# Kernel optimization log

Hardware: AMD Instinct MI355X
Metric: run time of the kernel (lower is better)

The kernel has to match this reference:

```python
import jax, jax.numpy as jnp
import numpy as np

VOCAB, EMBED, HIDDEN, T = 50257, 512, 1024, 2048

def setup_inputs() -> dict:
    key = jax.random.key(0)
    ks = jax.random.split(key, 7)
    s_e = 1.0 / np.sqrt(EMBED)
    s_h = 1.0 / np.sqrt(HIDDEN)
    return {
        "x": jax.random.randint(ks[0], (T,), 0, VOCAB),
        "emb": jax.random.normal(ks[1], (VOCAB, EMBED), dtype=jnp.float32),
        "W_xh": jax.random.uniform(ks[2], (HIDDEN, EMBED), minval=-s_e, maxval=s_e, dtype=jnp.float32),
        "W_hh": jax.random.uniform(ks[3], (HIDDEN, HIDDEN), minval=-s_h, maxval=s_h, dtype=jnp.float32),
        "b_hh": jax.random.uniform(ks[4], (HIDDEN,), minval=-s_h, maxval=s_h, dtype=jnp.float32),
        "W_out": jax.random.uniform(ks[5], (VOCAB, HIDDEN), minval=-s_h, maxval=s_h, dtype=jnp.float32),
        "b_out": jax.random.uniform(ks[6], (VOCAB,), minval=-s_h, maxval=s_h, dtype=jnp.float32),
    }

def reference(x, emb, W_xh, W_hh, b_hh, W_out, b_out):
    # embeds: [T, E]; precompute input projections for all steps (batched GEMM)
    embeds = emb[x]                      # [T, E]
    xp = embeds @ W_xh.T                 # [T, H]

    def step(h, xp_t):
        # h: [H]; nonlinear recurrence must be sequential
        h_new = jnp.tanh(xp_t + h @ W_hh.T + b_hh)
        return h_new, h_new

    h0 = jnp.zeros((HIDDEN,), dtype=xp.dtype)
    h_final, hs = jax.lax.scan(step, h0, xp)   # hs: [T, H]
    logits = hs @ W_out.T + b_out               # [T, VOCAB]
    return logits, h_final[None, :]
```

## Files before the change

### kernel.cpp

```cpp
#include <hip/hip_runtime.h>
#include <hip/hip_bf16.h>

#define VOCAB 50257
#define EMBED 512
#define HIDDEN 1024
#define TSEQ 2048
#define NPAD 50304
#define LOGITS_SIZE ((size_t)TSEQ * VOCAB)

#define OFF_XP   ((size_t)0)
#define OFF_HS   ((size_t)(TSEQ * HIDDEN * 4))
#define OFF_HP   (OFF_HS + (size_t)TSEQ * HIDDEN * 2)
#define OFF_WB   (OFF_HP + 16384 + 256)
#define WS_NEED_FULL (OFF_WB + (size_t)NPAD * HIDDEN * 2)

typedef short bf16x8 __attribute__((ext_vector_type(8)));
typedef float f32x4  __attribute__((ext_vector_type(4)));
typedef short short8 __attribute__((ext_vector_type(8)));

static __device__ __forceinline__ unsigned short f2bf(float f) {
    unsigned u = __float_as_uint(f);
    unsigned r = (u + 0x7fffu + ((u >> 16) & 1u)) >> 16;
    return (unsigned short)r;
}

__global__ __launch_bounds__(256, 2) void emb_xp_kernel(
    const int* __restrict__ x, const float* __restrict__ emb,
    const float* __restrict__ Wxh, float* __restrict__ xp)
{
    __shared__ float As[64][68];
    __shared__ float Bs[64][68];
    __shared__ int   xs[64];
    const int tid = threadIdx.x;
    const int t0 = blockIdx.y * 64, j0 = blockIdx.x * 64;
    if (tid < 64) xs[tid] = x[t0 + tid];
    __syncthreads();
    const int ty = tid >> 4, tx = tid & 15;
    float acc[4][4] = {};
    for (int kc = 0; kc < EMBED; kc += 64) {
        __syncthreads();
#pragma unroll
        for (int i = 0; i < 4; ++i) {
            int s = i * 256 + tid;
            int r = s >> 4, c4 = s & 15;
            *(float4*)&As[r][c4 * 4] = *(const float4*)&emb[(size_t)xs[r] * EMBED + kc + c4 * 4];
            *(float4*)&Bs[r][c4 * 4] = *(const float4*)&Wxh[(size_t)(j0 + r) * EMBED + kc + c4 * 4];
        }
        __syncthreads();
        for (int kk = 0; kk < 64; ++kk) {
            float a[4], b[4];
#pragma unroll
            for (int u = 0; u < 4; ++u) a[u] = As[ty + 16 * u][kk];
#pragma unroll
            for (int v = 0; v < 4; ++v) b[v] = Bs[tx + 16 * v][kk];
#pragma unroll
            for (int u = 0; u < 4; ++u)
#pragma unroll
                for (int v = 0; v < 4; ++v) acc[u][v] += a[u] * b[v];
        }
    }
#pragma unroll
    for (int u = 0; u < 4; ++u)
#pragma unroll
        for (int v = 0; v < 4; ++v)
            xp[(size_t)(t0 + ty + 16 * u) * HIDDEN + j0 + tx + 16 * v] = acc[u][v];
}

__global__ void conv_wout_kernel(const float* __restrict__ W, unsigned short* __restrict__ Wb)
{
    size_t i = (size_t)blockIdx.x * blockDim.x + threadIdx.x;
    size_t idx = i * 4;
    if (idx >= (size_t)NPAD * HIDDEN) return;
    size_t row = idx >> 10;
    float4 v = make_float4(0.f, 0.f, 0.f, 0.f);
    if (row < VOCAB) v = *(const float4*)&W[idx];
    ushort4 o = make_ushort4(f2bf(v.x), f2bf(v.y), f2bf(v.z), f2bf(v.w));
    *(ushort4*)&Wb[idx] = o;
}

#define RNN_WGS 256
__global__ __launch_bounds__(64, 1) void rnn_recur_kernel(
    const float* __restrict__ xp, const float* __restrict__ Whh,
    const float* __restrict__ bhh, unsigned long long* hpair ,
    unsigned short* __restrict__ hs_bf16, float* __restrict__ h_final)
{
    const int tid = threadIdx.x;
    const int j = blockIdx.x * 4 + (tid >> 4);
    const int k16 = tid & 15;

    float4 w4[16];
#pragma unroll
    for (int ii = 0; ii < 16; ++ii)
        w4[ii] = *(const float4*)&Whh[(size_t)j * HIDDEN + ii * 64 + k16 * 4];
#pragma unroll
    for (int ii = 0; ii < 16; ++ii)
        asm volatile("" : "+v"(w4[ii].x), "+v"(w4[ii].y), "+v"(w4[ii].z), "+v"(w4[ii].w));
    const float bj = bhh[j];

#pragma unroll 1
    for (int t = 0; t < TSEQ; ++t) {
        unsigned long long* hin  = hpair + ((t & 1) << 10);
        unsigned long long* hout = hpair + (((t + 1) & 1) << 10);
        const float xpv = xp[(size_t)t * HIDDEN + j];

        float hvf[64];
        for (;;) {
            int mn = 0x7fffffff;
#pragma unroll
            for (int ii = 0; ii < 16; ++ii) {
#pragma unroll
                for (int c = 0; c < 4; ++c) {
                    unsigned long long v = __hip_atomic_load(
                        &hin[ii * 64 + k16 * 4 + c],
                        __ATOMIC_RELAXED, __HIP_MEMORY_SCOPE_AGENT);
                    int tag = (int)(unsigned)(v >> 32);
                    mn = tag < mn ? tag : mn;
                    hvf[ii * 4 + c] = __uint_as_float((unsigned)v);
                }
            }
            if (__all(mn >= t)) break;
        }

        float sum = 0.f;
#pragma unroll
        for (int ii = 0; ii < 16; ++ii)
            sum += w4[ii].x * hvf[ii * 4 + 0] + w4[ii].y * hvf[ii * 4 + 1]
                 + w4[ii].z * hvf[ii * 4 + 2] + w4[ii].w * hvf[ii * 4 + 3];
        sum += __shfl_xor(sum, 1);
        sum += __shfl_xor(sum, 2);
        sum += __shfl_xor(sum, 4);
        sum += __shfl_xor(sum, 8);

        const float val = tanhf(sum + bj + xpv);
        if (k16 == 0) {
            unsigned long long pk = ((unsigned long long)(unsigned)(t + 1) << 32)
                                  | (unsigned long long)__float_as_uint(val);
            __hip_atomic_store(&hout[j], pk, __ATOMIC_RELAXED, __HIP_MEMORY_SCOPE_AGENT);
            hs_bf16[(size_t)t * HIDDEN + j] = f2bf(val);
            if (t == TSEQ - 1) h_final[j] = val;
        }
    }
}

template <bool PRE>
__global__ __launch_bounds__(256, 2) void out_gemm_kernel(
    const unsigned short* __restrict__ hs,
    const unsigned short* __restrict__ Wb,
    const float* __restrict__ Wf,
    const float* __restrict__ b_out,
    float* __restrict__ out)
{
    __shared__ short As[128 * 32];
    __shared__ short Bs[128 * 32];
    const int tid = threadIdx.x;
    const int wid = tid >> 6, lane = tid & 63;
    const int wm = wid >> 1, wn = wid & 1;
    const int l15 = lane & 15, quad = lane >> 4;
    const int m0 = blockIdx.y * 128, n0 = blockIdx.x * 128;

    f32x4 acc[4][4];
#pragma unroll
    for (int a = 0; a < 4; ++a)
#pragma unroll
        for (int b = 0; b < 4; ++b) acc[a][b] = (f32x4){0.f, 0.f, 0.f, 0.f};

    for (int k0 = 0; k0 < HIDDEN; k0 += 32) {
        __syncthreads();
#pragma unroll
        for (int i = 0; i < 2; ++i) {
            int ss = i * 256 + tid;
            int r = ss >> 2, c = ss & 3;
            short8 av = *(const short8*)(hs + (size_t)(m0 + r) * HIDDEN + k0 + c * 8);
            *(short8*)&As[r * 32 + c * 8] = av;
        }
        if (PRE) {
#pragma unroll
            for (int i = 0; i < 2; ++i) {
                int ss = i * 256 + tid;
                int r = ss >> 2, c = ss & 3;
                short8 bv = *(const short8*)(Wb + (size_t)(n0 + r) * HIDDEN + k0 + c * 8);
                *(short8*)&Bs[r * 32 + c * 8] = bv;
            }
        } else {
#pragma unroll
            for (int i = 0; i < 4; ++i) {
                int ss = i * 256 + tid;
                int r = ss >> 3, c4 = ss & 7;
                float4 v = make_float4(0.f, 0.f, 0.f, 0.f);
                if (n0 + r < VOCAB) v = *(const float4*)&Wf[(size_t)(n0 + r) * HIDDEN + k0 + c4 * 4];
                ushort4 u = make_ushort4(f2bf(v.x), f2bf(v.y), f2bf(v.z), f2bf(v.w));
                *(ushort4*)&Bs[r * 32 + c4 * 4] = u;
            }
        }
        __syncthreads();

        bf16x8 af[4], bfr[4];
#pragma unroll
        for (int mi = 0; mi < 4; ++mi)
            af[mi] = *(const bf16x8*)&As[(wm * 64 + mi * 16 + l15) * 32 + quad * 8];
#pragma unroll
        for (int ni = 0; ni < 4; ++ni)
            bfr[ni] = *(const bf16x8*)&Bs[(wn * 64 + ni * 16 + l15) * 32 + quad * 8];
#pragma unroll
        for (int mi = 0; mi < 4; ++mi)
#pragma unroll
            for (int ni = 0; ni < 4; ++ni)
                acc[mi][ni] = __builtin_amdgcn_mfma_f32_16x16x32_bf16(af[mi], bfr[ni], acc[mi][ni], 0, 0, 0);
    }

#pragma unroll
    for (int ni = 0; ni < 4; ++ni) {
        int n = n0 + wn * 64 + ni * 16 + l15;
        bool ok = n < VOCAB;
        float bias = ok ? b_out[n] : 0.f;
#pragma unroll
        for (int mi = 0; mi < 4; ++mi) {
            int mbase = m0 + wm * 64 + mi * 16 + quad * 4;
#pragma unroll
            for (int r = 0; r < 4; ++r) {
                if (ok) out[(size_t)(mbase + r) * VOCAB + n] = acc[mi][ni][r] + bias;
            }
        }
    }
}

extern "C" void kernel_launch(void* const* d_in, const int* in_sizes, int n_in,
                              void* d_out, int out_size, void* d_ws, size_t ws_size,
                              hipStream_t stream)
{
    const int*   x     = (const int*)d_in[0];
    const float* emb   = (const float*)d_in[1];
    const float* W_xh  = (const float*)d_in[2];
    const float* W_hh  = (const float*)d_in[3];
    const float* b_hh  = (const float*)d_in[4];
    const float* W_out = (const float*)d_in[5];
    const float* b_out = (const float*)d_in[6];
    float* out = (float*)d_out;
    char* ws = (char*)d_ws;

    float*              xp  = (float*)(ws + OFF_XP);
    unsigned short*     hsb = (unsigned short*)(ws + OFF_HS);
    unsigned long long* hp  = (unsigned long long*)(ws + OFF_HP);
    unsigned short*     Wb  = (unsigned short*)(ws + OFF_WB);

    hipMemsetAsync(ws + OFF_HP, 0, 16384, stream);

    emb_xp_kernel<<<dim3(HIDDEN / 64, TSEQ / 64), 256, 0, stream>>>(x, emb, W_xh, xp);

    const bool pre = ws_size >= WS_NEED_FULL;
    if (pre)
        conv_wout_kernel<<<(NPAD * HIDDEN / 4 + 255) / 256, 256, 0, stream>>>(W_out, Wb);

    rnn_recur_kernel<<<RNN_WGS, 64, 0, stream>>>(xp, W_hh, b_hh, hp, hsb,
                                                 out + LOGITS_SIZE);

    if (pre)
        out_gemm_kernel<true><<<dim3(NPAD / 128, TSEQ / 128), 256, 0, stream>>>(
            hsb, Wb, nullptr, b_out, out);
    else
        out_gemm_kernel<false><<<dim3(NPAD / 128, TSEQ / 128), 256, 0, stream>>>(
            hsb, nullptr, W_out, b_out, out);
}
```

Measured before the change: 6.010 ms.

## Share polled hidden state through LDS in larger RNN workgroups

The recurrence kernel now runs 64 workgroups of 256 threads instead of 256 workgroups of 64 threads, so each workgroup computes 16 hidden units. Each wave polls only a quarter of the tagged hidden vector with four atomic loads per lane and stores the values into shared memory. After a barrier, all waves read the full vector from LDS for the dot product. This is meant to cut the per-step global polling traffic and the spin-wait latency on the serial critical path. The cost is an extra __syncthreads per timestep and fewer workgroups taking part in the global handshake.

```diff
diff --git a/kernel.cpp b/kernel.cpp
--- a/kernel.cpp
+++ b/kernel.cpp
@@ -78,15 +78,18 @@
     *(ushort4*)&Wb[idx] = o;
 }
 
-#define RNN_WGS 256
-__global__ __launch_bounds__(64, 1) void rnn_recur_kernel(
+#define RNN_WGS 64
+__global__ __launch_bounds__(256, 1) void rnn_recur_kernel(
     const float* __restrict__ xp, const float* __restrict__ Whh,
     const float* __restrict__ bhh, unsigned long long* hpair ,
     unsigned short* __restrict__ hs_bf16, float* __restrict__ h_final)
 {
-    const int tid = threadIdx.x;
-    const int j = blockIdx.x * 4 + (tid >> 4);
-    const int k16 = tid & 15;
+    const int tid  = threadIdx.x;
+    const int lane = tid & 63;
+    const int wv   = tid >> 6;
+    const int jl   = tid >> 4;
+    const int j    = blockIdx.x * 16 + jl;
+    const int k16  = tid & 15;
 
     float4 w4[16];
 #pragma unroll
@@ -96,6 +99,9 @@
     for (int ii = 0; ii < 16; ++ii)
         asm volatile("" : "+v"(w4[ii].x), "+v"(w4[ii].y), "+v"(w4[ii].z), "+v"(w4[ii].w));
     const float bj = bhh[j];
+
+    __shared__ float hsm[HIDDEN];
+    const int pbase = wv * 256 + lane;
 
 #pragma unroll 1
     for (int t = 0; t < TSEQ; ++t) {
@@ -103,29 +109,31 @@
         unsigned long long* hout = hpair + (((t + 1) & 1) << 10);
         const float xpv = xp[(size_t)t * HIDDEN + j];
 
-        float hvf[64];
+        unsigned long long v0, v1, v2, v3;
         for (;;) {
-            int mn = 0x7fffffff;
-#pragma unroll
-            for (int ii = 0; ii < 16; ++ii) {
-#pragma unroll
-                for (int c = 0; c < 4; ++c) {
-                    unsigned long long v = __hip_atomic_load(
-                        &hin[ii * 64 + k16 * 4 + c],
-                        __ATOMIC_RELAXED, __HIP_MEMORY_SCOPE_AGENT);
-                    int tag = (int)(unsigned)(v >> 32);
-                    mn = tag < mn ? tag : mn;
-                    hvf[ii * 4 + c] = __uint_as_float((unsigned)v);
-                }
-            }
+            v0 = __hip_atomic_load(&hin[pbase],       __ATOMIC_RELAXED, __HIP_MEMORY_SCOPE_AGENT);
+            v1 = __hip_atomic_load(&hin[pbase +  64], __ATOMIC_RELAXED, __HIP_MEMORY_SCOPE_AGENT);
+            v2 = __hip_atomic_load(&hin[pbase + 128], __ATOMIC_RELAXED, __HIP_MEMORY_SCOPE_AGENT);
+            v3 = __hip_atomic_load(&hin[pbase + 192], __ATOMIC_RELAXED, __HIP_MEMORY_SCOPE_AGENT);
+            int t0 = (int)(unsigned)(v0 >> 32), t1 = (int)(unsigned)(v1 >> 32);
+            int t2 = (int)(unsigned)(v2 >> 32), t3 = (int)(unsigned)(v3 >> 32);
+            int mn = t0 < t1 ? t0 : t1;
+            int mn2 = t2 < t3 ? t2 : t3;
+            mn = mn < mn2 ? mn : mn2;
             if (__all(mn >= t)) break;
         }
+        hsm[pbase]       = __uint_as_float((unsigned)v0);
+        hsm[pbase +  64] = __uint_as_float((unsigned)v1);
+        hsm[pbase + 128] = __uint_as_float((unsigned)v2);
+        hsm[pbase + 192] = __uint_as_float((unsigned)v3);
+        __syncthreads();
 
         float sum = 0.f;
 #pragma unroll
-        for (int ii = 0; ii < 16; ++ii)
-            sum += w4[ii].x * hvf[ii * 4 + 0] + w4[ii].y * hvf[ii * 4 + 1]
-                 + w4[ii].z * hvf[ii * 4 + 2] + w4[ii].w * hvf[ii * 4 + 3];
+        for (int ii = 0; ii < 16; ++ii) {
+            float4 h4 = *(const float4*)&hsm[ii * 64 + k16 * 4];
+            sum += w4[ii].x * h4.x + w4[ii].y * h4.y + w4[ii].z * h4.z + w4[ii].w * h4.w;
+        }
         sum += __shfl_xor(sum, 1);
         sum += __shfl_xor(sum, 2);
         sum += __shfl_xor(sum, 4);
@@ -251,8 +259,8 @@
     if (pre)
         conv_wout_kernel<<<(NPAD * HIDDEN / 4 + 255) / 256, 256, 0, stream>>>(W_out, Wb);
 
-    rnn_recur_kernel<<<RNN_WGS, 64, 0, stream>>>(xp, W_hh, b_hh, hp, hsb,
-                                                 out + LOGITS_SIZE);
+    rnn_recur_kernel<<<RNN_WGS, 256, 0, stream>>>(xp, W_hh, b_hh, hp, hsb,
+                                                  out + LOGITS_SIZE);
 
     if (pre)
         out_gemm_kernel<true><<<dim3(NPAD / 128, TSEQ / 128), 256, 0, stream>>>(
```

After: 5.026 ms. 16.4% less time.
